# Kernel optimization log

Hardware: AMD Instinct MI355X
Metric: run time of the kernel (lower is better)

Reference implementation:

```python
import jax, jax.numpy as jnp
import numpy as np

EPS_NORM = 1e-12  # torch F.normalize eps
EPS_BN = 1e-5     # torch BatchNorm default eps


def l2norm(v, axis=-1):
    n = jnp.sqrt(jnp.sum(v * v, axis=axis, keepdims=True))
    return v / jnp.maximum(n, EPS_NORM)


def setup_inputs() -> dict:
    key = jax.random.key(0)
    k1, k2 = jax.random.split(key, 2)
    N, C, D, M, K = 4, 8, 196, 128, 64
    x = jax.random.normal(k1, (N, C, D, M), dtype=jnp.float32)
    # centroids ~ U[0,1) as in torch.rand
    centroids = jax.random.uniform(k2, (K, M), dtype=jnp.float32)
    alpha = 1.0
    # _init_params: conv.weight = 2*alpha*centroids (1x1 conv), conv.bias = -alpha*||centroids||
    conv_w = 2.0 * alpha * centroids            # (K, M)
    conv_b = -alpha * jnp.linalg.norm(centroids, axis=1)  # (K,)
    gamma = jnp.ones((C,), dtype=jnp.float32)   # BatchNorm3d(8) affine init
    beta = jnp.zeros((C,), dtype=jnp.float32)
    return {"x": x, "conv_w": conv_w, "conv_b": conv_b,
            "centroids": centroids, "gamma": gamma, "beta": beta}


def reference(x, conv_w, conv_b, centroids, gamma, beta):
    # x: (N, C, D, M) with M = descriptor dim, C must equal 8 (BatchNorm3d(8))
    xn = l2norm(x, axis=-1)  # descriptor-wise L2 norm (normalize_input=True)
    # 1x1 conv over channel axis M -> K cluster logits: (N, K, C, D)
    logits = jnp.einsum('ncdm,km->nkcd', xn, conv_w) + conv_b[None, :, None, None]
    soft_assign = jax.nn.softmax(logits, axis=1)  # over clusters K
    # residual: (N, K, C, D, M)
    residual = xn[:, None, :, :, :] - centroids[None, :, None, None, :]
    residual = residual * soft_assign[..., None]
    # permute to (N, C, D, K, M), intra-normalize over descriptor dim
    vlad = jnp.transpose(residual, (0, 2, 3, 1, 4))
    vlad = l2norm(vlad, axis=-1)
    # BatchNorm3d(8), training mode: stats over (N, D, K, M) per channel C
    mean = jnp.mean(vlad, axis=(0, 2, 3, 4), keepdims=True)
    var = jnp.mean((vlad - mean) ** 2, axis=(0, 2, 3, 4), keepdims=True)
    vlad = (vlad - mean) / jnp.sqrt(var + EPS_BN)
    vlad = vlad * gamma[None, :, None, None, None] + beta[None, :, None, None, None]
    N, C, D, K, M = vlad.shape
    vlad = vlad.reshape(N, C, D, K * M)
    return l2norm(vlad, axis=-1)
```

## Files before the change

### kernel.cpp

```cpp
#include <hip/hip_runtime.h>

#define NB 4
#define CB 8
#define DB 196
#define MBd 128
#define KBc 64
#define ROWS (NB*CB*DB)
#define RPB2 8
#define GRID2 (ROWS/RPB2)
#define RPB 7
#define GRID (ROWS/RPB)
#define CNTF 6422528.0f

typedef float floatx4 __attribute__((ext_vector_type(4)));

__device__ __forceinline__ float dot4(floatx4 a, floatx4 b){
    return fmaf(a.x,b.x, fmaf(a.y,b.y, fmaf(a.z,b.z, a.w*b.w)));
}

__global__ __launch_bounds__(256) void k_stats(const float* __restrict__ x,
                                               const float* __restrict__ cent,
                                               float* __restrict__ rn_ws,
                                               float* __restrict__ xrn_ws,
                                               float* __restrict__ sv_ws)
{
    __shared__ floatx4 ct4[32*65];
    __shared__ floatx4 xs4[RPB2*32];
    __shared__ float   svbuf[RPB2*65];

    const int t  = threadIdx.x;
    const int rb = blockIdx.x * RPB2;
    const floatx4* c4 = (const floatx4*)cent;
    const floatx4* xg = (const floatx4*)x;

#pragma unroll
    for (int i = 0; i < 8; ++i) {
        const int idx = i*256 + t;
        const int k = idx >> 5, m4 = idx & 31;
        ct4[m4*65 + k] = c4[idx];
    }
    xs4[t] = xg[rb*32 + t];
    __syncthreads();

    const int lane = t & 63, w = t >> 6;

    float ssck = 0.f, opck = 1.f;
#pragma unroll
    for (int m4 = 0; m4 < 32; ++m4) {
        const floatx4 cv = ct4[m4*65 + lane];
        ssck += (cv.x+cv.y)+(cv.z+cv.w);
        opck  = fmaf(cv.x,cv.x, fmaf(cv.y,cv.y, fmaf(cv.z,cv.z, fmaf(cv.w,cv.w, opck))));
    }

#pragma unroll
    for (int rr = 0; rr < 2; ++rr) {
        const int r   = w*2 + rr;
        const int row = rb + r;
        float d = 0.f, s2 = 0.f, sx = 0.f;
#pragma unroll
        for (int m4 = 0; m4 < 32; ++m4) {
            const floatx4 xv = xs4[r*32 + m4];
            const floatx4 cv = ct4[m4*65 + lane];
            d  = fmaf(xv.x,cv.x, fmaf(xv.y,cv.y, fmaf(xv.z,cv.z, fmaf(xv.w,cv.w, d))));
            s2 = fmaf(xv.x,xv.x, fmaf(xv.y,xv.y, fmaf(xv.z,xv.z, fmaf(xv.w,xv.w, s2))));
            sx += (xv.x+xv.y)+(xv.z+xv.w);
        }
        const float xrn = __builtin_amdgcn_rsqf(s2);
        const float rn  = __builtin_amdgcn_rsqf(fmaf(-2.f*xrn, d, opck));
        rn_ws[(size_t)row*KBc + lane] = rn;
        if (lane == 0) xrn_ws[row] = xrn;
        svbuf[r*65 + lane] = (sx*xrn - ssck) * rn;
    }
    __syncthreads();
    if (t < RPB2) {
        float s = 0.f;
#pragma unroll
        for (int j = 0; j < KBc; ++j) s += svbuf[t*65 + j];
        sv_ws[rb + t] = s;
    }
}

__global__ __launch_bounds__(256) void k_ab(const float* __restrict__ sv_ws,
                                            const float* __restrict__ gamma,
                                            const float* __restrict__ beta,
                                            float* __restrict__ ab_ws)
{
    __shared__ float red[256];
    const int c = blockIdx.x, t = threadIdx.x;
    float s = 0.f;
    for (int i = t; i < NB*DB; i += 256) {
        const int n = i / DB, d = i % DB;
        s += sv_ws[n*(CB*DB) + c*DB + d];
    }
    red[t] = s; __syncthreads();
#pragma unroll
    for (int sd = 128; sd >= 1; sd >>= 1) {
        if (t < sd) red[t] += red[t+sd];
        __syncthreads();
    }
    if (t == 0) {
        const float mean = red[0] / CNTF;
        const float var  = 0.0078125f - mean*mean;
        const float istd = __builtin_amdgcn_rsqf(var + 1e-5f);
        const float aa = istd * gamma[c];
        ab_ws[2*c]   = aa;
        ab_ws[2*c+1] = beta[c] - mean * aa;
    }
}

__global__ __launch_bounds__(256) void k_out(const float* __restrict__ x,
                                             const float* __restrict__ cent,
                                             const float* __restrict__ rn_ws,
                                             const float* __restrict__ xrn_ws,
                                             const float* __restrict__ sv_ws,
                                             const float* __restrict__ ab_ws,
                                             float* __restrict__ out)
{
    const int t   = threadIdx.x;
    const int row = blockIdx.x;
    const int c   = (row / DB) % CB;
    const int l = t & 63, w = t >> 6, li2 = l & 31, hi = l >> 5;
    const floatx4* c4 = (const floatx4*)cent;
    const floatx4* xg = (const floatx4*)x;

    const floatx4 xa  = xg[row*32 + li2];
    const float   xrn = xrn_ws[row];
    const float   SVr = sv_ws[row];
    const float   aa  = ab_ws[2*c];
    const float   bb  = ab_ws[2*c+1];
    floatx4 cv[8];
    float   rnv[8];
#pragma unroll
    for (int it = 0; it < 8; ++it) {
        const int k = it*8 + w*2 + hi;
        cv[it]  = c4[k*32 + li2];
        rnv[it] = rn_ws[(size_t)row*KBc + k];
    }

    const float rni = __builtin_amdgcn_rsqf(
        fmaf(2.f*aa*bb, SVr, fmaf(64.f*aa, aa, 8192.f*bb*bb)));
    const float f1  = aa * rni;
    const float c2v = bb * rni;
    const floatx4 va = xa * xrn;

    floatx4* outr = (floatx4*)out + (size_t)row*2048;
#pragma unroll
    for (int it = 0; it < 8; ++it) {
        const int k = it*8 + w*2 + hi;
        const float cc = f1 * rnv[it];
        floatx4 o1;
        o1.x = fmaf(va.x - cv[it].x, cc, c2v);
        o1.y = fmaf(va.y - cv[it].y, cc, c2v);
        o1.z = fmaf(va.z - cv[it].z, cc, c2v);
        o1.w = fmaf(va.w - cv[it].w, cc, c2v);
        outr[k*32 + li2] = o1;
    }
}

__global__ __launch_bounds__(256) void k_stats_f(const float* __restrict__ x,
                                                 const float* __restrict__ cent,
                                                 float* __restrict__ sv_ws,
                                                 float* __restrict__ partial,
                                                 float* __restrict__ opc_ws)
{
    __shared__ float cs[KBc*MBd];
    __shared__ float sopc[KBc];
    __shared__ float ssc[KBc];
    __shared__ float sp1[256], sp2[256];
    __shared__ float svp[RPB*4];
    __shared__ float sv7[RPB];

    const int t  = threadIdx.x;
    const int rb = blockIdx.x * RPB;
    const floatx4* c4 = (const floatx4*)cent;
    floatx4* cs4 = (floatx4*)cs;
#pragma unroll
    for (int i = 0; i < 8; ++i) cs4[i*256 + t] = c4[i*256 + t];
    __syncthreads();
    {
        const int kk = t >> 2, q = t & 3;
        const floatx4* crow = &cs4[kk*32 + q*8];
        float ps = 0.f, pc = 0.f;
#pragma unroll
        for (int f = 0; f < 8; ++f) { floatx4 v = crow[f]; ps += (v.x+v.y)+(v.z+v.w); pc += dot4(v,v); }
        sp1[t] = ps; sp2[t] = pc;
    }
    __syncthreads();
    if (t < KBc) {
        ssc[t]  = (sp1[4*t]+sp1[4*t+1])+(sp1[4*t+2]+sp1[4*t+3]);
        sopc[t] = 1.0f + ((sp2[4*t]+sp2[4*t+1])+(sp2[4*t+2]+sp2[4*t+3]));
    }
    __syncthreads();
    if (blockIdx.x == 0 && t < KBc) opc_ws[t] = sopc[t];

    const int l = t & 63, w = t >> 6, g = (l >> 4), li = l & 15;
    const floatx4* xg = (const floatx4*)x;
    for (int ri = 0; ri < RPB; ++ri) {
        const int row = rb + ri;
        floatx4 xa = xg[row*32 + li];
        floatx4 xb = xg[row*32 + 16 + li];
        float s2 = dot4(xa,xa) + dot4(xb,xb);
        float sx = ((xa.x+xa.y)+(xa.z+xa.w)) + ((xb.x+xb.y)+(xb.z+xb.w));
#pragma unroll
        for (int o = 8; o >= 1; o >>= 1) { s2 += __shfl_xor(s2,o,64); sx += __shfl_xor(sx,o,64); }
        const float xrn = __builtin_amdgcn_rsqf(s2);
        const float Sx  = sx * xrn;
        float sva = 0.f;
#pragma unroll
        for (int it = 0; it < 4; ++it) {
            const int k = it*16 + w*4 + g;
            float d = dot4(xa, cs4[k*32+li]) + dot4(xb, cs4[k*32+16+li]);
#pragma unroll
            for (int o = 8; o >= 1; o >>= 1) d += __shfl_xor(d,o,64);
            const float dn = xrn * d;
            const float rn = __builtin_amdgcn_rsqf(fmaf(-2.f, dn, sopc[k]));
            sva = fmaf(Sx - ssc[k], rn, sva);
        }
#pragma unroll
        for (int o = 32; o >= 1; o >>= 1) sva += __shfl_xor(sva,o,64);
        if (l == 0) svp[ri*4 + w] = sva * 0.0625f;
    }
    __syncthreads();
    if (t < RPB) {
        float s = (svp[4*t]+svp[4*t+1])+(svp[4*t+2]+svp[4*t+3]);
        sv_ws[rb + t] = s;
        sv7[t] = s;
    }
    __syncthreads();
    if (t == 0) {
        float s = 0.f;
#pragma unroll
        for (int i = 0; i < RPB; ++i) s += sv7[i];
        partial[blockIdx.x] = s;
    }
}

__global__ __launch_bounds__(256) void k_out_f(const float* __restrict__ x,
                                               const float* __restrict__ cent,
                                               const float* __restrict__ sv_ws,
                                               const float* __restrict__ partial,
                                               const float* __restrict__ opc_ws,
                                               const float* __restrict__ gamma,
                                               const float* __restrict__ beta,
                                               float* __restrict__ out)
{
    __shared__ float cs[KBc*MBd];
    __shared__ float sopc[KBc];
    __shared__ float sab[2];
    const int t  = threadIdx.x;
    const int rb = blockIdx.x * RPB;
    const int c  = (blockIdx.x / 28) % CB;
    const floatx4* c4 = (const floatx4*)cent;
    floatx4* cs4 = (floatx4*)cs;
#pragma unroll
    for (int i = 0; i < 8; ++i) cs4[i*256 + t] = c4[i*256 + t];
    if (t >= 64 && t < 128) sopc[t-64] = opc_ws[t-64];
    if (t < 64) {
        float s1 = 0.f;
        if (t < 56) {
            const int j0 = t, j1 = t + 56;
            const int b0 = (j0/28)*224 + c*28 + (j0%28);
            const int b1 = (j1/28)*224 + c*28 + (j1%28);
            s1 = partial[b0] + partial[b1];
        }
#pragma unroll
        for (int o = 32; o >= 1; o >>= 1) s1 += __shfl_xor(s1,o,64);
        if (t == 0) {
            const float mean = s1 / CNTF;
            const float var  = 0.0078125f - mean*mean;
            const float istd = __builtin_amdgcn_rsqf(var + 1e-5f);
            const float aa = istd * gamma[c];
            const float bb = beta[c] - mean * aa;
            sab[0] = aa; sab[1] = bb;
        }
    }
    __syncthreads();
    const float aa = sab[0], bb = sab[1];

    const int l = t & 63, w = t >> 6, g = (l >> 4), li = l & 15;
    const floatx4* xg = (const floatx4*)x;
    for (int ri = 0; ri < RPB; ++ri) {
        const int row = rb + ri;
        floatx4 xa = xg[row*32 + li];
        floatx4 xb = xg[row*32 + 16 + li];
        float s2 = dot4(xa,xa) + dot4(xb,xb);
#pragma unroll
        for (int o = 8; o >= 1; o >>= 1) s2 += __shfl_xor(s2,o,64);
        const float xrn = __builtin_amdgcn_rsqf(s2);
        const floatx4 va = xa * xrn, vb = xb * xrn;
        const float SVr = sv_ws[row];
        const float q   = fmaf(64.f*aa, aa, fmaf(2.f*aa*bb, SVr, 8192.f*bb*bb));
        const float rni = __builtin_amdgcn_rsqf(q);
        const float f1  = aa * rni;
        const float c2  = bb * rni;
        floatx4* outr = (floatx4*)out + (size_t)row*2048;
#pragma unroll
        for (int it = 0; it < 4; ++it) {
            const int k = it*16 + w*4 + g;
            const floatx4 cca = cs4[k*32+li];
            const floatx4 ccb = cs4[k*32+16+li];
            float d = dot4(va,cca) + dot4(vb,ccb);
#pragma unroll
            for (int o = 8; o >= 1; o >>= 1) d += __shfl_xor(d,o,64);
            const float rn = __builtin_amdgcn_rsqf(fmaf(-2.f, d, sopc[k]));
            const float cc = f1 * rn;
            floatx4 o1, o2;
            o1.x = fmaf(va.x - cca.x, cc, c2); o1.y = fmaf(va.y - cca.y, cc, c2);
            o1.z = fmaf(va.z - cca.z, cc, c2); o1.w = fmaf(va.w - cca.w, cc, c2);
            o2.x = fmaf(vb.x - ccb.x, cc, c2); o2.y = fmaf(vb.y - ccb.y, cc, c2);
            o2.z = fmaf(vb.z - ccb.z, cc, c2); o2.w = fmaf(vb.w - ccb.w, cc, c2);
            outr[k*32 + li]      = o1;
            outr[k*32 + 16 + li] = o2;
        }
    }
}

extern "C" void kernel_launch(void* const* d_in, const int* in_sizes, int n_in,
                              void* d_out, int out_size, void* d_ws, size_t ws_size,
                              hipStream_t stream)
{
    const float* x     = (const float*)d_in[0];
    const float* cent  = (const float*)d_in[3];
    const float* gamma = (const float*)d_in[4];
    const float* beta  = (const float*)d_in[5];
    float* out = (float*)d_out;

    const size_t need = (size_t)(ROWS*KBc + 2*ROWS + 16) * sizeof(float);
    if (ws_size >= need) {
        float* rn_ws   = (float*)d_ws;
        float* xrn_ws  = rn_ws + (size_t)ROWS*KBc;
        float* sv_ws   = xrn_ws + ROWS;
        float* ab_ws   = sv_ws + ROWS;
        hipLaunchKernelGGL(k_stats, dim3(GRID2), dim3(256), 0, stream,
                           x, cent, rn_ws, xrn_ws, sv_ws);
        hipLaunchKernelGGL(k_ab,    dim3(CB),    dim3(256), 0, stream,
                           sv_ws, gamma, beta, ab_ws);
        hipLaunchKernelGGL(k_out,   dim3(ROWS),  dim3(256), 0, stream,
                           x, cent, rn_ws, xrn_ws, sv_ws, ab_ws, out);
    } else {
        float* sv_ws   = (float*)d_ws;
        float* partial = sv_ws + ROWS;
        float* opc_ws  = partial + GRID;
        hipLaunchKernelGGL(k_stats_f, dim3(GRID), dim3(256), 0, stream,
                           x, cent, sv_ws, partial, opc_ws);
        hipLaunchKernelGGL(k_out_f,   dim3(GRID), dim3(256), 0, stream,
                           x, cent, sv_ws, partial, opc_ws, gamma, beta, out);
    }
}
```

Before: 59.76 us.

## Keep centroids in registers and precompute row norms cooperatively in k_stats

The stats kernel now holds each lane's centroid row in 32 vector registers instead of staging a transposed copy in shared memory. Each block processes 16 rows instead of 8. Per-row squared norms and sums are computed once by a parallel reduction instead of redundantly by every lane. This aims to cut shared-memory traffic and redundant ALU work in the dot-product loop, at the cost of heavy register pressure (128 VGPRs for centroids) and a halved grid size.

```diff
diff --git a/kernel.cpp b/kernel.cpp
--- a/kernel.cpp
+++ b/kernel.cpp
@@ -6,8 +6,8 @@
 #define MBd 128
 #define KBc 64
 #define ROWS (NB*CB*DB)
-#define RPB2 8
-#define GRID2 (ROWS/RPB2)
+#define RROWS 16
+#define GRID3 (ROWS/RROWS)
 #define RPB 7
 #define GRID (ROWS/RPB)
 #define CNTF 6422528.0f
@@ -24,58 +24,73 @@
                                                float* __restrict__ xrn_ws,
                                                float* __restrict__ sv_ws)
 {
-    __shared__ floatx4 ct4[32*65];
-    __shared__ floatx4 xs4[RPB2*32];
-    __shared__ float   svbuf[RPB2*65];
-
-    const int t  = threadIdx.x;
-    const int rb = blockIdx.x * RPB2;
+    __shared__ floatx4 xs4[RROWS*32];
+    __shared__ float p2[256], px[256];
+    __shared__ float rxrn[RROWS], rsxn[RROWS];
+    __shared__ float svbuf[RROWS*68];
+
+    const int t    = threadIdx.x;
+    const int rb   = blockIdx.x * RROWS;
+    const int lane = t & 63;
+    const int rs   = t >> 6;
     const floatx4* c4 = (const floatx4*)cent;
     const floatx4* xg = (const floatx4*)x;
 
-#pragma unroll
-    for (int i = 0; i < 8; ++i) {
-        const int idx = i*256 + t;
-        const int k = idx >> 5, m4 = idx & 31;
-        ct4[m4*65 + k] = c4[idx];
-    }
-    xs4[t] = xg[rb*32 + t];
-    __syncthreads();
-
-    const int lane = t & 63, w = t >> 6;
+    floatx4 creg[32];
+#pragma unroll
+    for (int m4 = 0; m4 < 32; ++m4) creg[m4] = c4[lane*32 + m4];
+
+    xs4[t]       = xg[rb*32 + t];
+    xs4[256 + t] = xg[rb*32 + 256 + t];
+    __syncthreads();
+
+    {
+        const int r = t >> 4, seg = t & 15;
+        const floatx4 a = xs4[r*32 + seg*2];
+        const floatx4 b = xs4[r*32 + seg*2 + 1];
+        p2[t] = dot4(a,a) + dot4(b,b);
+        px[t] = ((a.x+a.y)+(a.z+a.w)) + ((b.x+b.y)+(b.z+b.w));
+    }
+    __syncthreads();
+    if (t < RROWS) {
+        float s2 = 0.f, sx = 0.f;
+#pragma unroll
+        for (int j = 0; j < 16; ++j) { s2 += p2[t*16+j]; sx += px[t*16+j]; }
+        const float xrn = __builtin_amdgcn_rsqf(s2);
+        rxrn[t] = xrn;
+        rsxn[t] = sx * xrn;
+        xrn_ws[rb + t] = xrn;
+    }
 
     float ssck = 0.f, opck = 1.f;
 #pragma unroll
     for (int m4 = 0; m4 < 32; ++m4) {
-        const floatx4 cv = ct4[m4*65 + lane];
+        const floatx4 cv = creg[m4];
         ssck += (cv.x+cv.y)+(cv.z+cv.w);
         opck  = fmaf(cv.x,cv.x, fmaf(cv.y,cv.y, fmaf(cv.z,cv.z, fmaf(cv.w,cv.w, opck))));
     }
-
-#pragma unroll
-    for (int rr = 0; rr < 2; ++rr) {
-        const int r   = w*2 + rr;
-        const int row = rb + r;
-        float d = 0.f, s2 = 0.f, sx = 0.f;
+    __syncthreads();
+
+#pragma unroll
+    for (int rr = 0; rr < 4; ++rr) {
+        const int r = rs + rr*4;
+        float d = 0.f;
 #pragma unroll
         for (int m4 = 0; m4 < 32; ++m4) {
             const floatx4 xv = xs4[r*32 + m4];
-            const floatx4 cv = ct4[m4*65 + lane];
-            d  = fmaf(xv.x,cv.x, fmaf(xv.y,cv.y, fmaf(xv.z,cv.z, fmaf(xv.w,cv.w, d))));
-            s2 = fmaf(xv.x,xv.x, fmaf(xv.y,xv.y, fmaf(xv.z,xv.z, fmaf(xv.w,xv.w, s2))));
-            sx += (xv.x+xv.y)+(xv.z+xv.w);
-        }
-        const float xrn = __builtin_amdgcn_rsqf(s2);
+            d = fmaf(xv.x,creg[m4].x, fmaf(xv.y,creg[m4].y,
+                 fmaf(xv.z,creg[m4].z, fmaf(xv.w,creg[m4].w, d))));
+        }
+        const float xrn = rxrn[r];
         const float rn  = __builtin_amdgcn_rsqf(fmaf(-2.f*xrn, d, opck));
-        rn_ws[(size_t)row*KBc + lane] = rn;
-        if (lane == 0) xrn_ws[row] = xrn;
-        svbuf[r*65 + lane] = (sx*xrn - ssck) * rn;
-    }
-    __syncthreads();
-    if (t < RPB2) {
+        rn_ws[(size_t)(rb + r)*KBc + lane] = rn;
+        svbuf[r*68 + lane] = (rsxn[r] - ssck) * rn;
+    }
+    __syncthreads();
+    if (t < RROWS) {
         float s = 0.f;
 #pragma unroll
-        for (int j = 0; j < KBc; ++j) s += svbuf[t*65 + j];
+        for (int j = 0; j < KBc; ++j) s += svbuf[t*68 + j];
         sv_ws[rb + t] = s;
     }
 }
@@ -331,7 +346,7 @@
         float* xrn_ws  = rn_ws + (size_t)ROWS*KBc;
         float* sv_ws   = xrn_ws + ROWS;
         float* ab_ws   = sv_ws + ROWS;
-        hipLaunchKernelGGL(k_stats, dim3(GRID2), dim3(256), 0, stream,
+        hipLaunchKernelGGL(k_stats, dim3(GRID3), dim3(256), 0, stream,
                            x, cent, rn_ws, xrn_ws, sv_ws);
         hipLaunchKernelGGL(k_ab,    dim3(CB),    dim3(256), 0, stream,
                            sv_ws, gamma, beta, ab_ws);
```

Measured after the change: 51.96 us (median of 2 runs). 13.1% less time.
